# Performance work log

Measured on AMD Instinct MI355X. Metric: run time of the kernel, lower is better.

The kernel has to match this reference:

```python
import jax, jax.numpy as jnp
import numpy as np

N = 100000       # nodes
E = 1600000      # edges
EA = 7           # edge_attr_dim
H = 64           # hidden_dim
L = 32           # latent_dim
G = 512          # graphs in batch
C = 6            # num_classes


def _gin_conv(x, src, dst, edge_attr, We, be, W1, b1, W2, b2, eps):
    # GINE-style: message = relu(x_j + edge_proj), sum-aggregate at dst, then 2-layer MLP
    m = jax.nn.relu(x[src] + edge_attr @ We + be)            # [E, d_in]
    agg = jax.ops.segment_sum(m, dst, num_segments=x.shape[0])
    h = (1.0 + eps) * x + agg                                # [N, d_in]
    return jax.nn.relu(h @ W1 + b1) @ W2 + b2                # [N, H]


def setup_inputs() -> dict:
    key = jax.random.key(0)
    ks = jax.random.split(key, 24)
    s = 0.05
    inp = {
        "x": jax.random.normal(ks[0], (N,), jnp.float32),
        "edge_index": jax.random.randint(ks[1], (2, E), 0, N, jnp.int64),
        "edge_attr": jax.random.uniform(ks[2], (E, EA), jnp.float32),
        "batch": jnp.sort(jax.random.randint(ks[3], (N,), 0, G, jnp.int64)),
        # conv1 (input dim 1)
        "We1": jax.random.normal(ks[4], (EA, 1), jnp.float32) * s,
        "be1": jnp.zeros((1,), jnp.float32),
        "W11": jax.random.normal(ks[5], (1, H), jnp.float32) * s,
        "b11": jnp.zeros((H,), jnp.float32),
        "W12": jax.random.normal(ks[6], (H, H), jnp.float32) * s,
        "b12": jnp.zeros((H,), jnp.float32),
        "eps1": jnp.float32(0.0),
        # conv2 (input dim H)
        "We2": jax.random.normal(ks[7], (EA, H), jnp.float32) * s,
        "be2": jnp.zeros((H,), jnp.float32),
        "W21": jax.random.normal(ks[8], (H, H), jnp.float32) * s,
        "b21": jnp.zeros((H,), jnp.float32),
        "W22": jax.random.normal(ks[9], (H, H), jnp.float32) * s,
        "b22": jnp.zeros((H,), jnp.float32),
        "eps2": jnp.float32(0.0),
        # heads
        "Wmu": jax.random.normal(ks[10], (H, L), jnp.float32) * s,
        "bmu": jnp.zeros((L,), jnp.float32),
        "Wlv": jax.random.normal(ks[11], (H, L), jnp.float32) * s,
        "blv": jnp.zeros((L,), jnp.float32),
        "Wc": jax.random.normal(ks[12], (L, C), jnp.float32) * s,
        "bc": jnp.zeros((C,), jnp.float32),
    }
    return inp


def reference(x, edge_index, edge_attr, batch,
              We1, be1, W11, b11, W12, b12, eps1,
              We2, be2, W21, b21, W22, b22, eps2,
              Wmu, bmu, Wlv, blv, Wc, bc):
    src, dst = edge_index[0], edge_index[1]
    h = x.reshape(-1, 1)                                        # [N,1]
    h = jax.nn.relu(_gin_conv(h, src, dst, edge_attr, We1, be1, W11, b11, W12, b12, eps1))
    h = jax.nn.relu(_gin_conv(h, src, dst, edge_attr, We2, be2, W21, b21, W22, b22, eps2))
    mu = h @ Wmu + bmu                                          # [N,L]
    logvar = h @ Wlv + blv                                      # [N,L]
    # reparameterize (training path)
    noise = jax.random.normal(jax.random.key(42), mu.shape, mu.dtype)
    z = mu + noise * jnp.exp(0.5 * logvar)
    # global mean pool over graphs
    zsum = jax.ops.segment_sum(z, batch, num_segments=G)        # [G,L]
    cnt = jax.ops.segment_sum(jnp.ones((z.shape[0],), z.dtype), batch, num_segments=G)
    graph_emb = zsum / jnp.maximum(cnt, 1.0)[:, None]
    class_logits = graph_emb @ Wc + bc                          # [G,C]
    return (z, mu, logvar, class_logits)
```

## Files before the change

### kernel.cpp

```cpp
#include <hip/hip_runtime.h>
#include <stdint.h>

#define N_NODES 100000
#define N_EDGES 1600000
#define EAD 7
#define H 64
#define LAT 32
#define NG 512
#define NC 6

#define C1_NPB 32
#define C2_NPB 32
#define HD_NPB 64
#define NZ (N_NODES * LAT)
#define F4_PER_ARR (NZ / 4)

static_assert(N_NODES % C1_NPB == 0, "conv1_node grid exact");
static_assert(N_NODES % C2_NPB == 0, "conv2_node grid exact");

__device__ __forceinline__ void threefry2x32_42(uint32_t& x0, uint32_t& x1) {
    const uint32_t k0 = 0u, k1 = 42u;
    const uint32_t k2 = k0 ^ k1 ^ 0x1BD11BDAu;
    x0 += k0; x1 += k1;
#define TF_ROUND(r) { x0 += x1; x1 = (x1 << (r)) | (x1 >> (32 - (r))); x1 ^= x0; }
    TF_ROUND(13) TF_ROUND(15) TF_ROUND(26) TF_ROUND(6)
    x0 += k1; x1 += k2 + 1u;
    TF_ROUND(17) TF_ROUND(29) TF_ROUND(16) TF_ROUND(24)
    x0 += k2; x1 += k0 + 2u;
    TF_ROUND(13) TF_ROUND(15) TF_ROUND(26) TF_ROUND(6)
    x0 += k0; x1 += k1 + 3u;
    TF_ROUND(17) TF_ROUND(29) TF_ROUND(16) TF_ROUND(24)
    x0 += k1; x1 += k2 + 4u;
    TF_ROUND(13) TF_ROUND(15) TF_ROUND(26) TF_ROUND(6)
    x0 += k2; x1 += k0 + 5u;
#undef TF_ROUND
}

__device__ __forceinline__ float erfinv_f32(float x) {
    float w = -log1pf(-x * x);
    float p;
    if (w < 5.0f) {
        w = w - 2.5f;
        p = 2.81022636e-08f;
        p = fmaf(p, w, 3.43273939e-07f);
        p = fmaf(p, w, -3.5233877e-06f);
        p = fmaf(p, w, -4.39150654e-06f);
        p = fmaf(p, w, 0.00021858087f);
        p = fmaf(p, w, -0.00125372503f);
        p = fmaf(p, w, -0.00417768164f);
        p = fmaf(p, w, 0.246640727f);
        p = fmaf(p, w, 1.50140941f);
    } else {
        w = sqrtf(w) - 3.0f;
        p = -0.000200214257f;
        p = fmaf(p, w, 0.000100950558f);
        p = fmaf(p, w, 0.00134934322f);
        p = fmaf(p, w, -0.00367342844f);
        p = fmaf(p, w, 0.00573950773f);
        p = fmaf(p, w, -0.0076224613f);
        p = fmaf(p, w, 0.00943887047f);
        p = fmaf(p, w, 1.00167406f);
        p = fmaf(p, w, 2.83297682f);
    }
    return p * x;
}

__global__ void conv1_edge(const float* __restrict__ x, const int* __restrict__ src,
                           const int* __restrict__ dst, const float* __restrict__ ea,
                           const float* __restrict__ We1, const float* __restrict__ be1,
                           float* __restrict__ agg1) {
    int e = blockIdx.x * blockDim.x + threadIdx.x;
    if (e >= N_EDGES) return;
    float proj = be1[0];
#pragma unroll
    for (int k = 0; k < EAD; k++) proj = fmaf(ea[e * EAD + k], We1[k], proj);
    float m = x[src[e]] + proj;
    m = m > 0.0f ? m : 0.0f;
    atomicAdd(&agg1[dst[e]], m);
}

__global__ void conv1_node(const float* __restrict__ x, const float* __restrict__ agg1,
                           const float* __restrict__ W11, const float* __restrict__ b11,
                           const float* __restrict__ W12, const float* __restrict__ b12,
                           const float* __restrict__ eps1, float* __restrict__ hout) {
    __shared__ float sW12[H * H];
    __shared__ float st[4][H];
    int tid = threadIdx.x;
    for (int i = tid; i < H * H; i += 256) sW12[i] = W12[i];
    int sub = tid >> 6, lane = tid & 63;
    float eps = eps1[0];
    float w11 = W11[lane], bb11 = b11[lane], bb12 = b12[lane];
    __syncthreads();
#pragma unroll
    for (int it = 0; it < C1_NPB / 4; it++) {
        int n = blockIdx.x * C1_NPB + it * 4 + sub;
        float h1 = fmaf(eps, x[n], x[n]) + agg1[n];
        float t = fmaf(h1, w11, bb11);
        st[sub][lane] = t > 0.0f ? t : 0.0f;
        __syncthreads();
        float acc = bb12;
#pragma unroll
        for (int j = 0; j < H; j++) acc = fmaf(st[sub][j], sW12[j * H + lane], acc);
        hout[(size_t)n * H + lane] = acc > 0.0f ? acc : 0.0f;
        __syncthreads();
    }
}

__global__ void conv2_edge(const float* __restrict__ h, const int* __restrict__ src,
                           const int* __restrict__ dst, const float* __restrict__ ea,
                           const float* __restrict__ We2, const float* __restrict__ be2,
                           float* __restrict__ agg2) {
    int lane = threadIdx.x & 63;
    int e = (blockIdx.x * blockDim.x + threadIdx.x) >> 6;
    if (e >= N_EDGES) return;
    int s = src[e], d = dst[e];
    float proj = be2[lane];
#pragma unroll
    for (int k = 0; k < EAD; k++) proj = fmaf(ea[e * EAD + k], We2[k * H + lane], proj);
    float m = h[(size_t)s * H + lane] + proj;
    m = m > 0.0f ? m : 0.0f;
    atomicAdd(&agg2[(size_t)d * H + lane], m);
}

__global__ void conv2_node(const float* __restrict__ hin, const float* __restrict__ agg2,
                           const float* __restrict__ W21, const float* __restrict__ b21,
                           const float* __restrict__ W22, const float* __restrict__ b22,
                           const float* __restrict__ eps2, float* __restrict__ hout) {
    __shared__ float sW21[H * H], sW22[H * H];
    __shared__ float sh2[4][H], st[4][H];
    int tid = threadIdx.x;
    for (int i = tid; i < H * H; i += 256) { sW21[i] = W21[i]; sW22[i] = W22[i]; }
    int sub = tid >> 6, lane = tid & 63;
    float e = eps2[0];
    float bb21 = b21[lane], bb22 = b22[lane];
    __syncthreads();
#pragma unroll
    for (int it = 0; it < C2_NPB / 4; it++) {
        int n = blockIdx.x * C2_NPB + it * 4 + sub;
        float hv = hin[(size_t)n * H + lane];
        sh2[sub][lane] = fmaf(e, hv, hv) + agg2[(size_t)n * H + lane];
        __syncthreads();
        float acc = bb21;
#pragma unroll
        for (int j = 0; j < H; j++) acc = fmaf(sh2[sub][j], sW21[j * H + lane], acc);
        st[sub][lane] = acc > 0.0f ? acc : 0.0f;
        __syncthreads();
        acc = bb22;
#pragma unroll
        for (int j = 0; j < H; j++) acc = fmaf(st[sub][j], sW22[j * H + lane], acc);
        hout[(size_t)n * H + lane] = acc > 0.0f ? acc : 0.0f;
        __syncthreads();
    }
}

__global__ void heads_ml(const float* __restrict__ h,
                         const float* __restrict__ Wmu, const float* __restrict__ bmu,
                         const float* __restrict__ Wlv, const float* __restrict__ blv,
                         float* __restrict__ muws, float* __restrict__ lvws) {
    __shared__ float sWmu[H * LAT], sWlv[H * LAT];
    __shared__ float sh[8][H];
    int tid = threadIdx.x;
    for (int i = tid; i < H * LAT; i += 256) { sWmu[i] = Wmu[i]; sWlv[i] = Wlv[i]; }
    int sub = tid >> 5, lane = tid & 31;
    float bbmu = bmu[lane], bblv = blv[lane];
    __syncthreads();
    for (int it = 0; it < HD_NPB / 8; it++) {
        int base = blockIdx.x * HD_NPB + it * 8;
        if (base >= N_NODES) break;
        for (int i = tid; i < 8 * H; i += 256) {
            int nn = base + (i >> 6);
            if (nn < N_NODES) sh[i >> 6][i & 63] = h[(size_t)nn * H + (i & 63)];
        }
        __syncthreads();
        int n = base + sub;
        if (n < N_NODES) {
            float mu = bbmu, lv = bblv;
#pragma unroll
            for (int j = 0; j < H; j++) {
                float hv = sh[sub][j];
                mu = fmaf(hv, sWmu[j * LAT + lane], mu);
                lv = fmaf(hv, sWlv[j * LAT + lane], lv);
            }
            size_t o = (size_t)n * LAT + lane;
            muws[o] = mu; lvws[o] = lv;
        }
        __syncthreads();
    }
}

__global__ void heads_z(const float* __restrict__ muws, const float* __restrict__ lvws,
                        float* __restrict__ zws) {
    int i = blockIdx.x * blockDim.x + threadIdx.x;
    if (i >= NZ) return;
    float mu = muws[i], lv = lvws[i];
    uint32_t x0 = 0u, x1 = (uint32_t)i;
    threefry2x32_42(x0, x1);
    uint32_t bits = x0 ^ x1;
    float f = __uint_as_float((bits >> 9) | 0x3F800000u) - 1.0f;
    const float lo = -0.99999994f;
    float u = fmaxf(lo, fmaf(f, 2.0f, lo));
    float noise = 1.41421356237309515f * erfinv_f32(u);
    zws[i] = fmaf(noise, expf(0.5f * lv), mu);
}

__global__ void copyout_k(const float4* __restrict__ zs, const float4* __restrict__ ms,
                          const float4* __restrict__ ls, float4* __restrict__ out) {
    int i = blockIdx.x * blockDim.x + threadIdx.x;
    if (i < F4_PER_ARR) {
        out[i] = zs[i];
        out[F4_PER_ARR + i] = ms[i];
        out[2 * F4_PER_ARR + i] = ls[i];
    }
}

__global__ void pool_logits_k(const float4* __restrict__ z4, const int* __restrict__ batch,
                              const float* __restrict__ Wc, const float* __restrict__ bc,
                              float* __restrict__ out) {
    int g = blockIdx.x;
    int tid = threadIdx.x;
    int sub = tid >> 3, slot = tid & 7;
    __shared__ float4 acc4[32][8];
    __shared__ float emb[LAT];
    int lo = 0, hi = N_NODES;
    while (lo < hi) { int mid = (lo + hi) >> 1; if (batch[mid] < g) lo = mid + 1; else hi = mid; }
    int start = lo;
    hi = N_NODES;
    while (lo < hi) { int mid = (lo + hi) >> 1; if (batch[mid] < g + 1) lo = mid + 1; else hi = mid; }
    int end = lo;
    float4 a = make_float4(0.f, 0.f, 0.f, 0.f);
    for (int n = start + sub; n < end; n += 32) {
        float4 v = z4[(size_t)n * (LAT / 4) + slot];
        a.x += v.x; a.y += v.y; a.z += v.z; a.w += v.w;
    }
    acc4[sub][slot] = a;
    __syncthreads();
    if (tid < 8) {
        float4 s4 = acc4[0][tid];
        for (int k = 1; k < 32; k++) {
            s4.x += acc4[k][tid].x; s4.y += acc4[k][tid].y;
            s4.z += acc4[k][tid].z; s4.w += acc4[k][tid].w;
        }
        float invc = 1.0f / fmaxf((float)(end - start), 1.0f);
        emb[tid * 4 + 0] = s4.x * invc; emb[tid * 4 + 1] = s4.y * invc;
        emb[tid * 4 + 2] = s4.z * invc; emb[tid * 4 + 3] = s4.w * invc;
    }
    __syncthreads();
    if (tid < NC) {
        float r = bc[tid];
#pragma unroll
        for (int l = 0; l < LAT; l++) r = fmaf(emb[l], Wc[l * NC + tid], r);
        out[g * NC + tid] = r;
    }
}

extern "C" void kernel_launch(void* const* d_in, const int* in_sizes, int n_in,
                              void* d_out, int out_size, void* d_ws, size_t ws_size,
                              hipStream_t stream) {
    const float* x     = (const float*)d_in[0];
    const int*   ei    = (const int*)d_in[1];
    const float* ea    = (const float*)d_in[2];
    const int*   batch = (const int*)d_in[3];
    const float* We1   = (const float*)d_in[4];
    const float* be1   = (const float*)d_in[5];
    const float* W11   = (const float*)d_in[6];
    const float* b11   = (const float*)d_in[7];
    const float* W12   = (const float*)d_in[8];
    const float* b12   = (const float*)d_in[9];
    const float* eps1  = (const float*)d_in[10];
    const float* We2   = (const float*)d_in[11];
    const float* be2   = (const float*)d_in[12];
    const float* W21   = (const float*)d_in[13];
    const float* b21   = (const float*)d_in[14];
    const float* W22   = (const float*)d_in[15];
    const float* b22   = (const float*)d_in[16];
    const float* eps2  = (const float*)d_in[17];
    const float* Wmu   = (const float*)d_in[18];
    const float* bmu   = (const float*)d_in[19];
    const float* Wlv   = (const float*)d_in[20];
    const float* blv   = (const float*)d_in[21];
    const float* Wc    = (const float*)d_in[22];
    const float* bc    = (const float*)d_in[23];

    float* agg1 = (float*)d_ws;
    float* agg2 = agg1 + N_NODES;
    float* hA   = agg2 + (size_t)N_NODES * H;
    float* muws = agg2;
    float* lvws = agg2 + (size_t)NZ;
    float* zws  = hA;

    size_t zero_bytes = ((size_t)N_NODES + (size_t)N_NODES * H) * sizeof(float);
    hipMemsetAsync(d_ws, 0, zero_bytes, stream);

    const int* src = ei;
    const int* dst = ei + N_EDGES;

    conv1_edge<<<(N_EDGES + 255) / 256, 256, 0, stream>>>(x, src, dst, ea, We1, be1, agg1);
    conv1_node<<<N_NODES / C1_NPB, 256, 0, stream>>>(x, agg1, W11, b11, W12, b12, eps1, hA);
    conv2_edge<<<N_EDGES / 4, 256, 0, stream>>>(hA, src, dst, ea, We2, be2, agg2);
    conv2_node<<<N_NODES / C2_NPB, 256, 0, stream>>>(hA, agg2, W21, b21, W22, b22, eps2, hA);
    heads_ml<<<(N_NODES + HD_NPB - 1) / HD_NPB, 256, 0, stream>>>(
        hA, Wmu, bmu, Wlv, blv, muws, lvws);
    heads_z<<<(NZ + 255) / 256, 256, 0, stream>>>(muws, lvws, zws);
    copyout_k<<<(F4_PER_ARR + 255) / 256, 256, 0, stream>>>(
        (const float4*)zws, (const float4*)muws, (const float4*)lvws, (float4*)d_out);
    pool_logits_k<<<NG, 256, 0, stream>>>((const float4*)zws, batch, Wc, bc,
                                          (float*)d_out + 3 * (size_t)NZ);
}
```

Baseline: 765.3 us.

## Build CSR by destination and fuse gather-aggregate with node MLPs

Measured after the change: 1.127 ms. +47.3%, slower.

```diff
diff --git a/kernel.cpp b/kernel.cpp
--- a/kernel.cpp
+++ b/kernel.cpp
@@ -8,15 +8,16 @@
 #define LAT 32
 #define NG 512
 #define NC 6
-
-#define C1_NPB 32
-#define C2_NPB 32
+#define NZ (N_NODES * LAT)
+
+#define NB_SCAN 391
+#define NPW1 10
+#define NPW2 10
 #define HD_NPB 64
-#define NZ (N_NODES * LAT)
-#define F4_PER_ARR (NZ / 4)
-
-static_assert(N_NODES % C1_NPB == 0, "conv1_node grid exact");
-static_assert(N_NODES % C2_NPB == 0, "conv2_node grid exact");
+
+static_assert(N_NODES % (4 * NPW1) == 0, "conv1 grid exact");
+static_assert(N_NODES % (4 * NPW2) == 0, "conv2 grid exact");
+static_assert(N_EDGES % 256 == 0, "edge grid exact");
 
 __device__ __forceinline__ void threefry2x32_42(uint32_t& x0, uint32_t& x1) {
     const uint32_t k0 = 0u, k1 = 42u;
@@ -65,98 +66,223 @@
     return p * x;
 }
 
-__global__ void conv1_edge(const float* __restrict__ x, const int* __restrict__ src,
-                           const int* __restrict__ dst, const float* __restrict__ ea,
-                           const float* __restrict__ We1, const float* __restrict__ be1,
-                           float* __restrict__ agg1) {
+__global__ void hist_k(const int* __restrict__ dst, int* __restrict__ deg) {
+    int e = blockIdx.x * blockDim.x + threadIdx.x;
+    if (e < N_EDGES) atomicAdd(&deg[dst[e]], 1);
+}
+
+__global__ void scan1_k(const int* __restrict__ deg, int* __restrict__ bsum) {
+    __shared__ int sv[256];
+    int t = threadIdx.x, i = blockIdx.x * 256 + t;
+    sv[t] = (i < N_NODES) ? deg[i] : 0;
+    __syncthreads();
+    for (int o = 128; o > 0; o >>= 1) {
+        if (t < o) sv[t] += sv[t + o];
+        __syncthreads();
+    }
+    if (t == 0) bsum[blockIdx.x] = sv[0];
+}
+
+__global__ void scan2_k(int* __restrict__ bsum) {
+    __shared__ int sv[512];
+    int t = threadIdx.x;
+    int v = (t < NB_SCAN) ? bsum[t] : 0;
+    sv[t] = v;
+    __syncthreads();
+    for (int o = 1; o < 512; o <<= 1) {
+        int a = (t >= o) ? sv[t - o] : 0;
+        __syncthreads();
+        sv[t] += a;
+        __syncthreads();
+    }
+    if (t < NB_SCAN) bsum[t] = sv[t] - v;
+}
+
+__global__ void scan3_k(const int* __restrict__ deg, const int* __restrict__ bsum,
+                        int* __restrict__ off, int* __restrict__ cur) {
+    __shared__ int sv[256];
+    int t = threadIdx.x, i = blockIdx.x * 256 + t;
+    int v = (i < N_NODES) ? deg[i] : 0;
+    sv[t] = v;
+    __syncthreads();
+    for (int o = 1; o < 256; o <<= 1) {
+        int a = (t >= o) ? sv[t - o] : 0;
+        __syncthreads();
+        sv[t] += a;
+        __syncthreads();
+    }
+    if (i < N_NODES) {
+        int s = bsum[blockIdx.x] + sv[t] - v;
+        off[i] = s;
+        cur[i] = s;
+    }
+}
+
+__global__ void scatter_k(const float* __restrict__ x, const int* __restrict__ src,
+                          const int* __restrict__ dst, const float* __restrict__ ea,
+                          const float* __restrict__ We1, const float* __restrict__ be1,
+                          int* __restrict__ cur, int2* __restrict__ rec8,
+                          float* __restrict__ m1s) {
     int e = blockIdx.x * blockDim.x + threadIdx.x;
     if (e >= N_EDGES) return;
-    float proj = be1[0];
-#pragma unroll
-    for (int k = 0; k < EAD; k++) proj = fmaf(ea[e * EAD + k], We1[k], proj);
-    float m = x[src[e]] + proj;
+    int s = src[e], d = dst[e];
+    const float* ep = ea + (size_t)e * EAD;
+    float p = be1[0];
+#pragma unroll
+    for (int k = 0; k < EAD; k++) p = fmaf(ep[k], We1[k], p);
+    float m = x[s] + p;
     m = m > 0.0f ? m : 0.0f;
-    atomicAdd(&agg1[dst[e]], m);
-}
-
-__global__ void conv1_node(const float* __restrict__ x, const float* __restrict__ agg1,
-                           const float* __restrict__ W11, const float* __restrict__ b11,
-                           const float* __restrict__ W12, const float* __restrict__ b12,
-                           const float* __restrict__ eps1, float* __restrict__ hout) {
+    int pos = atomicAdd(&cur[d], 1);
+    rec8[pos] = make_int2(s, e);
+    m1s[pos] = m;
+}
+
+__global__ void conv1_fused(const float* __restrict__ x, const float* __restrict__ m1s,
+                            const int* __restrict__ off, const int* __restrict__ cur,
+                            const float* __restrict__ W11, const float* __restrict__ b11,
+                            const float* __restrict__ W12, const float* __restrict__ b12,
+                            const float* __restrict__ eps1, float* __restrict__ hA) {
     __shared__ float sW12[H * H];
-    __shared__ float st[4][H];
+    __shared__ float stg[4][H];
     int tid = threadIdx.x;
     for (int i = tid; i < H * H; i += 256) sW12[i] = W12[i];
-    int sub = tid >> 6, lane = tid & 63;
-    float eps = eps1[0];
-    float w11 = W11[lane], bb11 = b11[lane], bb12 = b12[lane];
-    __syncthreads();
-#pragma unroll
-    for (int it = 0; it < C1_NPB / 4; it++) {
-        int n = blockIdx.x * C1_NPB + it * 4 + sub;
-        float h1 = fmaf(eps, x[n], x[n]) + agg1[n];
-        float t = fmaf(h1, w11, bb11);
-        st[sub][lane] = t > 0.0f ? t : 0.0f;
-        __syncthreads();
-        float acc = bb12;
-#pragma unroll
-        for (int j = 0; j < H; j++) acc = fmaf(st[sub][j], sW12[j * H + lane], acc);
-        hout[(size_t)n * H + lane] = acc > 0.0f ? acc : 0.0f;
-        __syncthreads();
-    }
-}
-
-__global__ void conv2_edge(const float* __restrict__ h, const int* __restrict__ src,
-                           const int* __restrict__ dst, const float* __restrict__ ea,
-                           const float* __restrict__ We2, const float* __restrict__ be2,
-                           float* __restrict__ agg2) {
-    int lane = threadIdx.x & 63;
-    int e = (blockIdx.x * blockDim.x + threadIdx.x) >> 6;
-    if (e >= N_EDGES) return;
-    int s = src[e], d = dst[e];
-    float proj = be2[lane];
-#pragma unroll
-    for (int k = 0; k < EAD; k++) proj = fmaf(ea[e * EAD + k], We2[k * H + lane], proj);
-    float m = h[(size_t)s * H + lane] + proj;
-    m = m > 0.0f ? m : 0.0f;
-    atomicAdd(&agg2[(size_t)d * H + lane], m);
-}
-
-__global__ void conv2_node(const float* __restrict__ hin, const float* __restrict__ agg2,
-                           const float* __restrict__ W21, const float* __restrict__ b21,
-                           const float* __restrict__ W22, const float* __restrict__ b22,
-                           const float* __restrict__ eps2, float* __restrict__ hout) {
+    int w = tid >> 6, lane = tid & 63;
+    float rW11 = W11[lane], rb11 = b11[lane], rb12 = b12[lane], er = eps1[0];
+    __syncthreads();
+    int n0 = (blockIdx.x * 4 + w) * NPW1;
+    for (int ni = 0; ni < NPW1; ni++) {
+        int n = n0 + ni;
+        int g0 = off[n], g1 = cur[n];
+        float agg = 0.0f;
+        for (int j = g0 + lane; j < g1; j += 64) agg += m1s[j];
+#pragma unroll
+        for (int o = 32; o > 0; o >>= 1) agg += __shfl_xor(agg, o, 64);
+        float xv = x[n];
+        float h1 = fmaf(er, xv, xv) + agg;
+        float t = fmaf(h1, rW11, rb11);
+        t = t > 0.0f ? t : 0.0f;
+        stg[w][lane] = t;
+        float acc = rb12;
+#pragma unroll
+        for (int j = 0; j < H; j++) acc = fmaf(stg[w][j], sW12[j * H + lane], acc);
+        hA[(size_t)n * H + lane] = acc > 0.0f ? acc : 0.0f;
+    }
+}
+
+__global__ void conv2_fused(const float* __restrict__ hin, const int2* __restrict__ rec8,
+                            const float* __restrict__ ea,
+                            const int* __restrict__ off, const int* __restrict__ cur,
+                            const float* __restrict__ We2, const float* __restrict__ be2,
+                            const float* __restrict__ W21, const float* __restrict__ b21,
+                            const float* __restrict__ W22, const float* __restrict__ b22,
+                            const float* __restrict__ eps2, float* __restrict__ hB) {
     __shared__ float sW21[H * H], sW22[H * H];
-    __shared__ float sh2[4][H], st[4][H];
+    __shared__ float4 srec[4][64][2];
+    __shared__ float stg[4][H];
     int tid = threadIdx.x;
     for (int i = tid; i < H * H; i += 256) { sW21[i] = W21[i]; sW22[i] = W22[i]; }
-    int sub = tid >> 6, lane = tid & 63;
-    float e = eps2[0];
-    float bb21 = b21[lane], bb22 = b22[lane];
-    __syncthreads();
-#pragma unroll
-    for (int it = 0; it < C2_NPB / 4; it++) {
-        int n = blockIdx.x * C2_NPB + it * 4 + sub;
-        float hv = hin[(size_t)n * H + lane];
-        sh2[sub][lane] = fmaf(e, hv, hv) + agg2[(size_t)n * H + lane];
-        __syncthreads();
-        float acc = bb21;
-#pragma unroll
-        for (int j = 0; j < H; j++) acc = fmaf(sh2[sub][j], sW21[j * H + lane], acc);
-        st[sub][lane] = acc > 0.0f ? acc : 0.0f;
-        __syncthreads();
-        acc = bb22;
-#pragma unroll
-        for (int j = 0; j < H; j++) acc = fmaf(st[sub][j], sW22[j * H + lane], acc);
-        hout[(size_t)n * H + lane] = acc > 0.0f ? acc : 0.0f;
-        __syncthreads();
-    }
-}
-
-__global__ void heads_ml(const float* __restrict__ h,
-                         const float* __restrict__ Wmu, const float* __restrict__ bmu,
-                         const float* __restrict__ Wlv, const float* __restrict__ blv,
-                         float* __restrict__ muws, float* __restrict__ lvws) {
+    int w = tid >> 6, lane = tid & 63;
+    float rW[EAD];
+#pragma unroll
+    for (int k = 0; k < EAD; k++) rW[k] = We2[k * H + lane];
+    float rbe2 = be2[lane], rb21 = b21[lane], rb22 = b22[lane], er = eps2[0];
+    __syncthreads();
+
+    int n0 = (blockIdx.x * 4 + w) * NPW2;
+    int eend = cur[n0 + NPW2 - 1];
+    int sbase = -(1 << 30);
+
+    auto restage = [&](int g) {
+        sbase = g;
+        int cnt = eend - g; cnt = cnt > 64 ? 64 : cnt;
+        float a0 = 0, a1 = 0, a2 = 0, a3 = 0, a4 = 0, a5 = 0, a6 = 0;
+        int s = 0;
+        if (lane < cnt) {
+            int2 r = rec8[g + lane];
+            s = r.x;
+            const float* ep = ea + (size_t)r.y * EAD;
+            a0 = ep[0]; a1 = ep[1]; a2 = ep[2]; a3 = ep[3];
+            a4 = ep[4]; a5 = ep[5]; a6 = ep[6];
+        }
+        srec[w][lane][0] = make_float4(a0, a1, a2, a3);
+        srec[w][lane][1] = make_float4(a4, a5, a6, __int_as_float(s));
+    };
+
+    for (int ni = 0; ni < NPW2; ni++) {
+        int n = n0 + ni;
+        int g = off[n], gend = cur[n];
+        float acc = 0.0f;
+        while (g + 4 <= gend) {
+            if (g + 4 > sbase + 64) restage(g);
+            int b = g - sbase;
+            float4 A0 = srec[w][b + 0][0], B0 = srec[w][b + 0][1];
+            float4 A1 = srec[w][b + 1][0], B1 = srec[w][b + 1][1];
+            float4 A2 = srec[w][b + 2][0], B2 = srec[w][b + 2][1];
+            float4 A3 = srec[w][b + 3][0], B3 = srec[w][b + 3][1];
+            int s0 = __builtin_amdgcn_readfirstlane(__float_as_int(B0.w));
+            int s1 = __builtin_amdgcn_readfirstlane(__float_as_int(B1.w));
+            int s2 = __builtin_amdgcn_readfirstlane(__float_as_int(B2.w));
+            int s3 = __builtin_amdgcn_readfirstlane(__float_as_int(B3.w));
+            float hv0 = hin[(size_t)s0 * H + lane];
+            float hv1 = hin[(size_t)s1 * H + lane];
+            float hv2 = hin[(size_t)s2 * H + lane];
+            float hv3 = hin[(size_t)s3 * H + lane];
+            float p0 = rbe2, p1 = rbe2, p2 = rbe2, p3 = rbe2;
+            p0 = fmaf(A0.x, rW[0], p0); p0 = fmaf(A0.y, rW[1], p0);
+            p0 = fmaf(A0.z, rW[2], p0); p0 = fmaf(A0.w, rW[3], p0);
+            p0 = fmaf(B0.x, rW[4], p0); p0 = fmaf(B0.y, rW[5], p0);
+            p0 = fmaf(B0.z, rW[6], p0);
+            p1 = fmaf(A1.x, rW[0], p1); p1 = fmaf(A1.y, rW[1], p1);
+            p1 = fmaf(A1.z, rW[2], p1); p1 = fmaf(A1.w, rW[3], p1);
+            p1 = fmaf(B1.x, rW[4], p1); p1 = fmaf(B1.y, rW[5], p1);
+            p1 = fmaf(B1.z, rW[6], p1);
+            p2 = fmaf(A2.x, rW[0], p2); p2 = fmaf(A2.y, rW[1], p2);
+            p2 = fmaf(A2.z, rW[2], p2); p2 = fmaf(A2.w, rW[3], p2);
+            p2 = fmaf(B2.x, rW[4], p2); p2 = fmaf(B2.y, rW[5], p2);
+            p2 = fmaf(B2.z, rW[6], p2);
+            p3 = fmaf(A3.x, rW[0], p3); p3 = fmaf(A3.y, rW[1], p3);
+            p3 = fmaf(A3.z, rW[2], p3); p3 = fmaf(A3.w, rW[3], p3);
+            p3 = fmaf(B3.x, rW[4], p3); p3 = fmaf(B3.y, rW[5], p3);
+            p3 = fmaf(B3.z, rW[6], p3);
+            acc += fmaxf(hv0 + p0, 0.0f);
+            acc += fmaxf(hv1 + p1, 0.0f);
+            acc += fmaxf(hv2 + p2, 0.0f);
+            acc += fmaxf(hv3 + p3, 0.0f);
+            g += 4;
+        }
+        while (g < gend) {
+            if (g >= sbase + 64) restage(g);
+            int b = g - sbase;
+            float4 A = srec[w][b][0], B = srec[w][b][1];
+            int s = __builtin_amdgcn_readfirstlane(__float_as_int(B.w));
+            float hv = hin[(size_t)s * H + lane];
+            float p = rbe2;
+            p = fmaf(A.x, rW[0], p); p = fmaf(A.y, rW[1], p);
+            p = fmaf(A.z, rW[2], p); p = fmaf(A.w, rW[3], p);
+            p = fmaf(B.x, rW[4], p); p = fmaf(B.y, rW[5], p);
+            p = fmaf(B.z, rW[6], p);
+            acc += fmaxf(hv + p, 0.0f);
+            g++;
+        }
+        float hself = hin[(size_t)n * H + lane];
+        float h2 = fmaf(er, hself, hself) + acc;
+        stg[w][lane] = h2;
+        float t = rb21;
+#pragma unroll
+        for (int j = 0; j < H; j++) t = fmaf(stg[w][j], sW21[j * H + lane], t);
+        t = t > 0.0f ? t : 0.0f;
+        stg[w][lane] = t;
+        float o2 = rb22;
+#pragma unroll
+        for (int j = 0; j < H; j++) o2 = fmaf(stg[w][j], sW22[j * H + lane], o2);
+        hB[(size_t)n * H + lane] = o2 > 0.0f ? o2 : 0.0f;
+    }
+}
+
+__global__ void heads_mlz(const float* __restrict__ hB,
+                          const float* __restrict__ Wmu, const float* __restrict__ bmu,
+                          const float* __restrict__ Wlv, const float* __restrict__ blv,
+                          float* __restrict__ out) {
     __shared__ float sWmu[H * LAT], sWlv[H * LAT];
     __shared__ float sh[8][H];
     int tid = threadIdx.x;
@@ -169,7 +295,7 @@
         if (base >= N_NODES) break;
         for (int i = tid; i < 8 * H; i += 256) {
             int nn = base + (i >> 6);
-            if (nn < N_NODES) sh[i >> 6][i & 63] = h[(size_t)nn * H + (i & 63)];
+            if (nn < N_NODES) sh[i >> 6][i & 63] = hB[(size_t)nn * H + (i & 63)];
         }
         __syncthreads();
         int n = base + sub;
@@ -181,35 +307,20 @@
                 mu = fmaf(hv, sWmu[j * LAT + lane], mu);
                 lv = fmaf(hv, sWlv[j * LAT + lane], lv);
             }
-            size_t o = (size_t)n * LAT + lane;
-            muws[o] = mu; lvws[o] = lv;
-        }
-        __syncthreads();
-    }
-}
-
-__global__ void heads_z(const float* __restrict__ muws, const float* __restrict__ lvws,
-                        float* __restrict__ zws) {
-    int i = blockIdx.x * blockDim.x + threadIdx.x;
-    if (i >= NZ) return;
-    float mu = muws[i], lv = lvws[i];
-    uint32_t x0 = 0u, x1 = (uint32_t)i;
-    threefry2x32_42(x0, x1);
-    uint32_t bits = x0 ^ x1;
-    float f = __uint_as_float((bits >> 9) | 0x3F800000u) - 1.0f;
-    const float lo = -0.99999994f;
-    float u = fmaxf(lo, fmaf(f, 2.0f, lo));
-    float noise = 1.41421356237309515f * erfinv_f32(u);
-    zws[i] = fmaf(noise, expf(0.5f * lv), mu);
-}
-
-__global__ void copyout_k(const float4* __restrict__ zs, const float4* __restrict__ ms,
-                          const float4* __restrict__ ls, float4* __restrict__ out) {
-    int i = blockIdx.x * blockDim.x + threadIdx.x;
-    if (i < F4_PER_ARR) {
-        out[i] = zs[i];
-        out[F4_PER_ARR + i] = ms[i];
-        out[2 * F4_PER_ARR + i] = ls[i];
+            int i = n * LAT + lane;
+            uint32_t x0 = 0u, x1 = (uint32_t)i;
+            threefry2x32_42(x0, x1);
+            uint32_t bits = x0 ^ x1;
+            float f = __uint_as_float((bits >> 9) | 0x3F800000u) - 1.0f;
+            const float lo = -0.99999994f;
+            float u = fmaxf(lo, fmaf(f, 2.0f, lo));
+            float noise = 1.41421356237309515f * erfinv_f32(u);
+            float z = fmaf(noise, expf(0.5f * lv), mu);
+            out[i] = z;
+            out[NZ + i] = mu;
+            out[2 * NZ + i] = lv;
+        }
+        __syncthreads();
     }
 }
 
@@ -281,28 +392,32 @@
     const float* Wc    = (const float*)d_in[22];
     const float* bc    = (const float*)d_in[23];
 
-    float* agg1 = (float*)d_ws;
-    float* agg2 = agg1 + N_NODES;
-    float* hA   = agg2 + (size_t)N_NODES * H;
-    float* muws = agg2;
-    float* lvws = agg2 + (size_t)NZ;
-    float* zws  = hA;
-
-    size_t zero_bytes = ((size_t)N_NODES + (size_t)N_NODES * H) * sizeof(float);
-    hipMemsetAsync(d_ws, 0, zero_bytes, stream);
+    int*   deg  = (int*)d_ws;
+    int*   off  = deg + N_NODES;
+    int*   cur  = off + N_NODES;
+    int*   bsum = cur + N_NODES;
+    int2*  rec8 = (int2*)(bsum + 512);
+    float* m1s  = (float*)(rec8 + N_EDGES);
+    float* hB   = m1s + N_EDGES;
+    float* hA   = (float*)d_out;
+    float* outf = (float*)d_out;
+
+    hipMemsetAsync(deg, 0, N_NODES * sizeof(int), stream);
 
     const int* src = ei;
     const int* dst = ei + N_EDGES;
 
-    conv1_edge<<<(N_EDGES + 255) / 256, 256, 0, stream>>>(x, src, dst, ea, We1, be1, agg1);
-    conv1_node<<<N_NODES / C1_NPB, 256, 0, stream>>>(x, agg1, W11, b11, W12, b12, eps1, hA);
-    conv2_edge<<<N_EDGES / 4, 256, 0, stream>>>(hA, src, dst, ea, We2, be2, agg2);
-    conv2_node<<<N_NODES / C2_NPB, 256, 0, stream>>>(hA, agg2, W21, b21, W22, b22, eps2, hA);
-    heads_ml<<<(N_NODES + HD_NPB - 1) / HD_NPB, 256, 0, stream>>>(
-        hA, Wmu, bmu, Wlv, blv, muws, lvws);
-    heads_z<<<(NZ + 255) / 256, 256, 0, stream>>>(muws, lvws, zws);
-    copyout_k<<<(F4_PER_ARR + 255) / 256, 256, 0, stream>>>(
-        (const float4*)zws, (const float4*)muws, (const float4*)lvws, (float4*)d_out);
-    pool_logits_k<<<NG, 256, 0, stream>>>((const float4*)zws, batch, Wc, bc,
-                                          (float*)d_out + 3 * (size_t)NZ);
-}
+    hist_k<<<N_EDGES / 256, 256, 0, stream>>>(dst, deg);
+    scan1_k<<<NB_SCAN, 256, 0, stream>>>(deg, bsum);
+    scan2_k<<<1, 512, 0, stream>>>(bsum);
+    scan3_k<<<NB_SCAN, 256, 0, stream>>>(deg, bsum, off, cur);
+    scatter_k<<<N_EDGES / 256, 256, 0, stream>>>(x, src, dst, ea, We1, be1, cur, rec8, m1s);
+    conv1_fused<<<N_NODES / (4 * NPW1), 256, 0, stream>>>(
+        x, m1s, off, cur, W11, b11, W12, b12, eps1, hA);
+    conv2_fused<<<N_NODES / (4 * NPW2), 256, 0, stream>>>(
+        hA, rec8, ea, off, cur, We2, be2, W21, b21, W22, b22, eps2, hB);
+    heads_mlz<<<(N_NODES + HD_NPB - 1) / HD_NPB, 256, 0, stream>>>(
+        hB, Wmu, bmu, Wlv, blv, outf);
+    pool_logits_k<<<NG, 256, 0, stream>>>((const float4*)outf, batch, Wc, bc,
+                                          outf + 3 * (size_t)NZ);
+}
```
